# Optimization experiments

Measured on AMD Instinct MI355X. Metric: run time of the kernel, lower is better.

The kernel has to match this reference:

```python
import jax, jax.numpy as jnp
import numpy as np

ALPHA = 0.1        # axis_aligned_projection threshold
NEG_INF = -1e30    # large negative used for masking (softmax-equivalent to -inf)


def axis_aligned_projection(x, alpha=ALPHA):
    x_abs = jnp.abs(x)
    max_vals = jnp.max(x_abs, axis=-1, keepdims=True)
    axis_weights = jnp.where(x_abs >= alpha * max_vals, x_abs, 0.0)
    return axis_weights * jnp.sign(x)


def setup_inputs() -> dict:
    key = jax.random.key(0)
    kq, kk, kv = jax.random.split(key, 3)
    B, L, H, E = 4, 2048, 8, 64
    S, D = L, E
    queries = jax.random.normal(kq, (B, L, H, E), dtype=jnp.float32)
    keys = jax.random.normal(kk, (B, S, H, E), dtype=jnp.float32)
    values = jax.random.normal(kv, (B, S, H, D), dtype=jnp.float32)
    # TriangularCausalMask: True strictly above the diagonal -> masked out
    causal = jnp.triu(jnp.ones((L, S), dtype=jnp.bool_), k=1)
    attn_mask = jnp.broadcast_to(causal[None, None], (B, 1, L, S))
    return {"queries": queries, "keys": keys, "values": values, "attn_mask": attn_mask}


def reference(queries, keys, values, attn_mask):
    B, L, H, E = queries.shape
    scale = 1.0 / jnp.sqrt(jnp.float32(E))
    q = axis_aligned_projection(queries)
    k = axis_aligned_projection(keys)
    # [B,H,L,S] dense scores (the module materializes the full matrix)
    scores = jnp.einsum('blhe,bshe->bhls', q, k)
    scores = jnp.where(attn_mask, NEG_INF, scores)
    A = jax.nn.softmax(scale * scores, axis=-1)  # dropout is identity in eval mode
    V = jnp.einsum('bhls,bshd->blhd', A, values)
    return V
```

## Files before the change

### kernel.cpp

```cpp
#include <hip/hip_runtime.h>
#include <hip/hip_bf16.h>
#include <stdint.h>

#define B_ 4
#define L_ 2048
#define H_ 8
#define E_ 64
#define ALPHA 0.1f
#define LOG2E 1.44269504088896f
#define QSCALE (0.125f * LOG2E)
#define KSTR 72

typedef float f32x4 __attribute__((ext_vector_type(4)));
typedef short bf16x8 __attribute__((ext_vector_type(8)));
typedef short bf16x4 __attribute__((ext_vector_type(4)));
typedef uint32_t u32;
typedef unsigned short u16;
typedef u32 u32x2 __attribute__((ext_vector_type(2)));

__device__ __forceinline__ u16 f2bf(float f) {
    u32 x = __builtin_bit_cast(u32, f);
    u32 r = x + 0x7fffu + ((x >> 16) & 1u);
    return (u16)(r >> 16);
}

__device__ __forceinline__ u32 pk2bf(float a, float b) {
    u32 ua = __builtin_bit_cast(u32, a) + 0x8000u;
    u32 ub = __builtin_bit_cast(u32, b) + 0x8000u;
    return (ua >> 16) | (ub & 0xffff0000u);
}

__device__ __forceinline__ f32x4 mfma16x16x16bf16(bf16x4 a, bf16x4 b, f32x4 c) {
#if __has_builtin(__builtin_amdgcn_mfma_f32_16x16x16bf16_1k)
    return __builtin_amdgcn_mfma_f32_16x16x16bf16_1k(a, b, c, 0, 0, 0);
#elif __has_builtin(__builtin_amdgcn_mfma_f32_16x16x16_bf16)
    return __builtin_amdgcn_mfma_f32_16x16x16_bf16(a, b, c, 0, 0, 0);
#else
    f32x4 d;
    asm volatile("v_mfma_f32_16x16x16_bf16 %0, %1, %2, %3"
                 : "=v"(d) : "v"(a), "v"(b), "v"(c));
    return d;
#endif
}

__device__ __forceinline__ void dma16(const u16* g, u16* l) {
    __builtin_amdgcn_global_load_lds(
        (const __attribute__((address_space(1))) void*)g,
        (__attribute__((address_space(3))) void*)l, 16, 0, 0);
}

__global__ __launch_bounds__(256) void prep_kernel(const float* __restrict__ qin,
                                                   const float* __restrict__ kin,
                                                   const float* __restrict__ vin,
                                                   u16* __restrict__ qp,
                                                   u16* __restrict__ kp,
                                                   u16* __restrict__ vt) {
    __shared__ u16 tile[64][66];
    if (blockIdx.x < 4096) {
        const int RG = (B_ * L_ * H_) / 8;
        int wave = threadIdx.x >> 6, lane = threadIdx.x & 63;
        int g = blockIdx.x * 4 + wave;
        const float* src;
        u16* dst;
        int gr, ostr;
        float sc;
        if (g < RG) { src = qin; dst = qp; gr = g; sc = QSCALE; ostr = 64; }
        else        { src = kin; dst = kp; gr = g - RG; sc = 1.0f; ostr = KSTR; }

        int rig = lane >> 3;
        int c = (lane & 7) * 4;
        int row = gr * 8 + rig;

        const float* rp = src + (size_t)row * 64;
        float4 v0 = *(const float4*)(rp + c);
        float4 v1 = *(const float4*)(rp + c + 32);
        float f[8] = {v0.x, v0.y, v0.z, v0.w, v1.x, v1.y, v1.z, v1.w};

        float mx = 0.f;
#pragma unroll
        for (int i = 0; i < 8; ++i) mx = fmaxf(mx, fabsf(f[i]));
#pragma unroll
        for (int m = 1; m < 8; m <<= 1) mx = fmaxf(mx, __shfl_xor(mx, m));
        float thr = ALPHA * mx;

        u16 o[8];
#pragma unroll
        for (int i = 0; i < 8; ++i)
            o[i] = (fabsf(f[i]) >= thr) ? f2bf(f[i] * sc) : (u16)0;

        int b = row >> 14;
        int l = (row >> 3) & (L_ - 1);
        int h = row & 7;
        u16* orow = dst + ((size_t)(b * H_ + h) * L_ + l) * ostr;
        uint2 p0 = {(u32)o[0] | ((u32)o[1] << 16), (u32)o[2] | ((u32)o[3] << 16)};
        uint2 p1 = {(u32)o[4] | ((u32)o[5] << 16), (u32)o[6] | ((u32)o[7] << 16)};
        *(uint2*)(orow + c) = p0;
        *(uint2*)(orow + c + 32) = p1;
    } else {
        int bx = blockIdx.x - 4096;
        int bh = bx >> 5, sblk = bx & 31;
        int b = bh >> 3, h = bh & 7;
        int t = threadIdx.x;
        int s0 = sblk * 64;

#pragma unroll
        for (int p = 0; p < 2; ++p) {
            int sl = p * 32 + (t >> 3);
            int c = (t & 7) * 4;
            const float* rp = vin + (((size_t)(b * L_ + s0 + sl)) * H_ + h) * 64;
            float4 a = *(const float4*)(rp + c);
            float4 bb = *(const float4*)(rp + c + 32);
            u32* d0 = (u32*)&tile[sl][c];
            d0[0] = (u32)f2bf(a.x) | ((u32)f2bf(a.y) << 16);
            d0[1] = (u32)f2bf(a.z) | ((u32)f2bf(a.w) << 16);
            u32* d1 = (u32*)&tile[sl][c + 32];
            d1[0] = (u32)f2bf(bb.x) | ((u32)f2bf(bb.y) << 16);
            d1[1] = (u32)f2bf(bb.z) | ((u32)f2bf(bb.w) << 16);
        }
        __syncthreads();
#pragma unroll
        for (int p = 0; p < 2; ++p) {
            int d = p * 32 + (t >> 3);
            int sc2 = (t & 7) * 8;
            u16 o[8];
#pragma unroll
            for (int i = 0; i < 8; ++i) o[i] = tile[sc2 + i][d];
            uint4 val;
            val.x = (u32)o[0] | ((u32)o[1] << 16);
            val.y = (u32)o[2] | ((u32)o[3] << 16);
            val.z = (u32)o[4] | ((u32)o[5] << 16);
            val.w = (u32)o[6] | ((u32)o[7] << 16);
            *(uint4*)(vt + ((size_t)(bh * 32 + sblk) * 64 + d) * KSTR + sc2) = val;
        }
    }
}

__global__ __launch_bounds__(256, 4) void flash_kernel(const u16* __restrict__ Qp,
                                                       const u16* __restrict__ Kp,
                                                       const u16* __restrict__ Vt,
                                                       float* __restrict__ out) {
    __shared__ u16 kbuf[2][64 * KSTR];
    __shared__ u16 vbuf[2][64 * KSTR];
    int t = threadIdx.x;
    int wave = t >> 6, lane = t & 63;
    int bh = blockIdx.x & 31;
    int r5 = blockIdx.x >> 5;
    int g = r5 & 7, kr = r5 >> 3;
    int qq = (kr == 0) ? (31 - g) : (kr == 1) ? (16 + g) : (kr == 2) ? (15 - g) : g;
    int lo = lane & 15, quad = lane >> 4;
    int q0 = qq * 64 + wave * 16;
    int b = bh >> 3, h = bh & 7;

    const u16* kTiles = Kp + (size_t)bh * L_ * KSTR;
    const u16* vTiles = Vt + (size_t)bh * 32 * 64 * KSTR;

    auto stage = [&](int sb, int buf) {
        const u16* kg = kTiles + (size_t)sb * KSTR;
        const u16* vg = vTiles + (size_t)(sb >> 6) * 64 * KSTR;
        u16* kl = kbuf[buf];
        u16* vl = vbuf[buf];
        for (int i = wave; i < 18; i += 4) {
            if (i < 9) dma16(kg + i * 512 + lane * 8, kl + i * 512);
            else       dma16(vg + (i - 9) * 512 + lane * 8, vl + (i - 9) * 512);
        }
    };

    const u16* qbase = Qp + ((size_t)bh * L_ + q0 + lo) * 64 + quad * 8;
    bf16x8 aQ0 = *(const bf16x8*)(qbase);
    bf16x8 aQ1 = *(const bf16x8*)(qbase + 32);

    f32x4 o[4];
#pragma unroll
    for (int ni = 0; ni < 4; ++ni) o[ni] = (f32x4){0.f, 0.f, 0.f, 0.f};
    float ls = 0.f;

    auto frag_proc = [&](const u16* ks, const u16* vs, int sub, bool diag) {
        bf16x8 k0 = *(const bf16x8*)(ks + (sub * 16 + lo) * KSTR + quad * 8);
        bf16x8 k1 = *(const bf16x8*)(ks + (sub * 16 + lo) * KSTR + 32 + quad * 8);
        f32x4 S = {0.f, 0.f, 0.f, 0.f};
        S = __builtin_amdgcn_mfma_f32_16x16x32_bf16(k0, aQ0, S, 0, 0, 0);
        S = __builtin_amdgcn_mfma_f32_16x16x32_bf16(k1, aQ1, S, 0, 0, 0);

        bf16x4 vf[4];
#pragma unroll
        for (int ni = 0; ni < 4; ++ni)
            vf[ni] = *(const bf16x4*)(vs + (ni * 16 + lo) * KSTR + sub * 16 + quad * 4);

        float P[4];
#pragma unroll
        for (int r = 0; r < 4; ++r) {
            float e = __builtin_amdgcn_exp2f(S[r]);
            P[r] = (diag && (quad * 4 + r > lo)) ? 0.f : e;
        }
        ls += (P[0] + P[1]) + (P[2] + P[3]);
        u32x2 pk = {pk2bf(P[0], P[1]), pk2bf(P[2], P[3])};
        bf16x4 aP = __builtin_bit_cast(bf16x4, pk);
#pragma unroll
        for (int ni = 0; ni < 4; ++ni)
            o[ni] = mfma16x16x16bf16(aP, vf[ni], o[ni]);
    };

    stage(0, 0);
    __syncthreads();

    for (int kt = 0; kt < qq; ++kt) {
        int cur = kt & 1;
        stage((kt + 1) << 6, cur ^ 1);
        const u16* ks = kbuf[cur];
        const u16* vs = vbuf[cur];
#pragma unroll
        for (int sub = 0; sub < 4; ++sub) frag_proc(ks, vs, sub, false);
        __syncthreads();
    }

    {
        int cur = qq & 1;
        const u16* ks = kbuf[cur];
        const u16* vs = vbuf[cur];
        for (int sub = 0; sub < wave; ++sub) frag_proc(ks, vs, sub, false);
        frag_proc(ks, vs, wave, true);
    }

    ls += __shfl_xor(ls, 16);
    ls += __shfl_xor(ls, 32);
#pragma unroll
    for (int r = 0; r < 4; ++r) {
        float lr = __shfl(ls, quad * 4 + r);
        float inv = 1.0f / lr;
        int q = q0 + quad * 4 + r;
        float* ob = out + (((size_t)(b * L_ + q)) * H_ + h) * 64 + lo;
        ob[0]  = o[0][r] * inv;
        ob[16] = o[1][r] * inv;
        ob[32] = o[2][r] * inv;
        ob[48] = o[3][r] * inv;
    }
}

extern "C" void kernel_launch(void* const* d_in, const int* in_sizes, int n_in,
                              void* d_out, int out_size, void* d_ws, size_t ws_size,
                              hipStream_t stream) {
    const float* q = (const float*)d_in[0];
    const float* k = (const float*)d_in[1];
    const float* v = (const float*)d_in[2];
    float* out = (float*)d_out;

    const size_t QSZ = (size_t)B_ * H_ * L_ * 64;
    const size_t KSZ = (size_t)B_ * H_ * L_ * KSTR;
    u16* qp = (u16*)d_ws;
    u16* kp = qp + QSZ;
    u16* vt = kp + KSZ;

    prep_kernel<<<5120, 256, 0, stream>>>(q, k, v, qp, kp, vt);
    flash_kernel<<<1024, 256, 0, stream>>>(qp, kp, vt, out);
}
```

Measured before the change: 170.2 us.

## Replace padded K/V LDS rows with XOR-swizzled unpadded layout

Drops the 72-element row padding for K and transposed V in both the workspace and LDS, and instead XOR-swizzles the 8- and 4-element column chunks at write time in the prep kernel. The flash kernel's reads apply the matching swizzle. This cuts global and LDS traffic by the unused padding and shrinks the DMA loop from 18 to 16 chunks while still avoiding LDS bank conflicts. The risk is that the swizzle on either the write or the read side is slightly wrong, which would corrupt results.

```diff
diff --git a/kernel.cpp b/kernel.cpp
--- a/kernel.cpp
+++ b/kernel.cpp
@@ -9,7 +9,7 @@
 #define ALPHA 0.1f
 #define LOG2E 1.44269504088896f
 #define QSCALE (0.125f * LOG2E)
-#define KSTR 72
+
 
 typedef float f32x4 __attribute__((ext_vector_type(4)));
 typedef short bf16x8 __attribute__((ext_vector_type(8)));
@@ -62,13 +62,15 @@
         int g = blockIdx.x * 4 + wave;
         const float* src;
         u16* dst;
-        int gr, ostr;
+        int gr;
         float sc;
-        if (g < RG) { src = qin; dst = qp; gr = g; sc = QSCALE; ostr = 64; }
-        else        { src = kin; dst = kp; gr = g - RG; sc = 1.0f; ostr = KSTR; }
+        bool isq;
+        if (g < RG) { src = qin; dst = qp; gr = g; sc = QSCALE; isq = true; }
+        else        { src = kin; dst = kp; gr = g - RG; sc = 1.0f; isq = false; }
 
         int rig = lane >> 3;
-        int c = (lane & 7) * 4;
+        int j = lane & 7;
+        int c = j * 4;
         int row = gr * 8 + rig;
 
         const float* rp = src + (size_t)row * 64;
@@ -91,11 +93,20 @@
         int b = row >> 14;
         int l = (row >> 3) & (L_ - 1);
         int h = row & 7;
-        u16* orow = dst + ((size_t)(b * H_ + h) * L_ + l) * ostr;
+        int e0, e1;
+        if (isq) {
+            e0 = c;
+            e1 = c + 32;
+        } else {
+            int l7 = l & 7;
+            e0 = (((j >> 1) ^ l7) << 3) + ((j & 1) << 2);
+            e1 = ((((j >> 1) + 4) ^ l7) << 3) + ((j & 1) << 2);
+        }
+        u16* orow = dst + ((size_t)(b * H_ + h) * L_ + l) * 64;
         uint2 p0 = {(u32)o[0] | ((u32)o[1] << 16), (u32)o[2] | ((u32)o[3] << 16)};
         uint2 p1 = {(u32)o[4] | ((u32)o[5] << 16), (u32)o[6] | ((u32)o[7] << 16)};
-        *(uint2*)(orow + c) = p0;
-        *(uint2*)(orow + c + 32) = p1;
+        *(uint2*)(orow + e0) = p0;
+        *(uint2*)(orow + e1) = p1;
     } else {
         int bx = blockIdx.x - 4096;
         int bh = bx >> 5, sblk = bx & 31;
@@ -121,16 +132,20 @@
 #pragma unroll
         for (int p = 0; p < 2; ++p) {
             int d = p * 32 + (t >> 3);
-            int sc2 = (t & 7) * 8;
+            int c16 = t & 7;
+            int sc2 = c16 * 8;
             u16 o[8];
 #pragma unroll
             for (int i = 0; i < 8; ++i) o[i] = tile[sc2 + i][d];
+            u32 w0 = (u32)o[0] | ((u32)o[1] << 16);
+            u32 w1 = (u32)o[2] | ((u32)o[3] << 16);
+            u32 w2 = (u32)o[4] | ((u32)o[5] << 16);
+            u32 w3 = (u32)o[6] | ((u32)o[7] << 16);
             uint4 val;
-            val.x = (u32)o[0] | ((u32)o[1] << 16);
-            val.y = (u32)o[2] | ((u32)o[3] << 16);
-            val.z = (u32)o[4] | ((u32)o[5] << 16);
-            val.w = (u32)o[6] | ((u32)o[7] << 16);
-            *(uint4*)(vt + ((size_t)(bh * 32 + sblk) * 64 + d) * KSTR + sc2) = val;
+            if (d & 1) { val.x = w2; val.y = w3; val.z = w0; val.w = w1; }
+            else       { val.x = w0; val.y = w1; val.z = w2; val.w = w3; }
+            int pc = c16 ^ ((d >> 1) & 7);
+            *(uint4*)(vt + ((size_t)(bh * 32 + sblk) * 64 + d) * 64 + pc * 8) = val;
         }
     }
 }
@@ -139,8 +154,8 @@
                                                        const u16* __restrict__ Kp,
                                                        const u16* __restrict__ Vt,
                                                        float* __restrict__ out) {
-    __shared__ u16 kbuf[2][64 * KSTR];
-    __shared__ u16 vbuf[2][64 * KSTR];
+    __shared__ u16 kbuf[2][64 * 64];
+    __shared__ u16 vbuf[2][64 * 64];
     int t = threadIdx.x;
     int wave = t >> 6, lane = t & 63;
     int bh = blockIdx.x & 31;
@@ -148,20 +163,24 @@
     int g = r5 & 7, kr = r5 >> 3;
     int qq = (kr == 0) ? (31 - g) : (kr == 1) ? (16 + g) : (kr == 2) ? (15 - g) : g;
     int lo = lane & 15, quad = lane >> 4;
+    int lo7 = lo & 7;
     int q0 = qq * 64 + wave * 16;
     int b = bh >> 3, h = bh & 7;
 
-    const u16* kTiles = Kp + (size_t)bh * L_ * KSTR;
-    const u16* vTiles = Vt + (size_t)bh * 32 * 64 * KSTR;
+    int kc0 = (quad ^ lo7) << 3;
+    int kc1 = ((quad + 4) ^ lo7) << 3;
+
+    const u16* kTiles = Kp + (size_t)bh * L_ * 64;
+    const u16* vTiles = Vt + (size_t)bh * 32 * 64 * 64;
 
     auto stage = [&](int sb, int buf) {
-        const u16* kg = kTiles + (size_t)sb * KSTR;
-        const u16* vg = vTiles + (size_t)(sb >> 6) * 64 * KSTR;
+        const u16* kg = kTiles + (size_t)sb * 64;
+        const u16* vg = vTiles + (size_t)(sb >> 6) * 64 * 64;
         u16* kl = kbuf[buf];
         u16* vl = vbuf[buf];
-        for (int i = wave; i < 18; i += 4) {
-            if (i < 9) dma16(kg + i * 512 + lane * 8, kl + i * 512);
-            else       dma16(vg + (i - 9) * 512 + lane * 8, vl + (i - 9) * 512);
+        for (int i = wave; i < 16; i += 4) {
+            if (i < 8) dma16(kg + i * 512 + lane * 8, kl + i * 512);
+            else       dma16(vg + (i - 8) * 512 + lane * 8, vl + (i - 8) * 512);
         }
     };
 
@@ -175,16 +194,18 @@
     float ls = 0.f;
 
     auto frag_proc = [&](const u16* ks, const u16* vs, int sub, bool diag) {
-        bf16x8 k0 = *(const bf16x8*)(ks + (sub * 16 + lo) * KSTR + quad * 8);
-        bf16x8 k1 = *(const bf16x8*)(ks + (sub * 16 + lo) * KSTR + 32 + quad * 8);
+        const u16* krow = ks + ((sub * 16 + lo) << 6);
+        bf16x8 k0 = *(const bf16x8*)(krow + kc0);
+        bf16x8 k1 = *(const bf16x8*)(krow + kc1);
         f32x4 S = {0.f, 0.f, 0.f, 0.f};
         S = __builtin_amdgcn_mfma_f32_16x16x32_bf16(k0, aQ0, S, 0, 0, 0);
         S = __builtin_amdgcn_mfma_f32_16x16x32_bf16(k1, aQ1, S, 0, 0, 0);
 
+        int vsw = ((sub * 4 + quad) ^ lo) << 2;
         bf16x4 vf[4];
 #pragma unroll
         for (int ni = 0; ni < 4; ++ni)
-            vf[ni] = *(const bf16x4*)(vs + (ni * 16 + lo) * KSTR + sub * 16 + quad * 4);
+            vf[ni] = *(const bf16x4*)(vs + ((ni * 16 + lo) << 6) + vsw);
 
         float P[4];
 #pragma unroll
@@ -245,10 +266,9 @@
     float* out = (float*)d_out;
 
     const size_t QSZ = (size_t)B_ * H_ * L_ * 64;
-    const size_t KSZ = (size_t)B_ * H_ * L_ * KSTR;
     u16* qp = (u16*)d_ws;
     u16* kp = qp + QSZ;
-    u16* vt = kp + KSZ;
+    u16* vt = kp + QSZ;
 
     prep_kernel<<<5120, 256, 0, stream>>>(q, k, v, qp, kp, vt);
     flash_kernel<<<1024, 256, 0, stream>>>(qp, kp, vt, out);
```

After: 163.8 us. -3.8%, faster.
